# Optimization experiments

Hardware: AMD Instinct MI355X
Metric: run time of the kernel (lower is better)

The kernel has to match this reference:

```python
import jax, jax.numpy as jnp
import numpy as np

N_NODES = 50000
N_EDGES = 1600000
IN_DIM = 128
HID = 128
SHARED = 64
N_GRAPHS = 2048


def setup_inputs() -> dict:
    key = jax.random.key(0)
    ks = jax.random.split(key, 16)
    x = jax.random.normal(ks[0], (N_NODES, IN_DIM), dtype=jnp.float32)
    edge_index = jax.random.randint(ks[1], (2, N_EDGES), 0, N_NODES, dtype=jnp.int64)
    batch = jnp.sort(jax.random.randint(ks[2], (N_NODES,), 0, N_GRAPHS, dtype=jnp.int64))

    def lin(k, fan_in, fan_out):
        bound = 1.0 / np.sqrt(fan_in)
        kw, kb = jax.random.split(k)
        W = jax.random.uniform(kw, (fan_in, fan_out), minval=-bound, maxval=bound, dtype=jnp.float32)
        b = jax.random.uniform(kb, (fan_out,), minval=-bound, maxval=bound, dtype=jnp.float32)
        return W, b

    W1a, b1a = lin(ks[3], IN_DIM, HID)
    W1b, b1b = lin(ks[4], HID, HID)
    W2a, b2a = lin(ks[5], HID, HID)
    W2b, b2b = lin(ks[6], HID, HID)
    Ws, bs = lin(ks[7], HID, SHARED)
    WlS, blS = lin(ks[8], SHARED, 1)
    WlP, blP = lin(ks[9], SHARED, 1)
    WnR, bnR = lin(ks[10], SHARED, 1)
    return dict(x=x, edge_index=edge_index, batch=batch,
                W1a=W1a, b1a=b1a, W1b=W1b, b1b=b1b,
                W2a=W2a, b2a=b2a, W2b=W2b, b2b=b2b,
                Ws=Ws, bs=bs, WlS=WlS, blS=blS, WlP=WlP, blP=blP, WnR=WnR, bnR=bnR)


def gin_conv(x, src, dst, Wa, ba, Wb, bb):
    # GINConv (eps=0): h_i = MLP(x_i + sum_{j->i} x_j)
    agg = jax.ops.segment_sum(x[src], dst, num_segments=N_NODES)
    h = x + agg
    h = jax.nn.relu(h @ Wa + ba)
    return h @ Wb + bb


def reference(x, edge_index, batch, W1a, b1a, W1b, b1b, W2a, b2a, W2b, b2b,
              Ws, bs, WlS, blS, WlP, blP, WnR, bnR):
    src, dst = edge_index[0], edge_index[1]
    h = jax.nn.relu(gin_conv(x, src, dst, W1a, b1a, W1b, b1b))
    h = jax.nn.relu(gin_conv(h, src, dst, W2a, b2a, W2b, b2b))
    # global mean pool over graph ids
    sums = jax.ops.segment_sum(h, batch, num_segments=N_GRAPHS)
    counts = jax.ops.segment_sum(jnp.ones((h.shape[0],), h.dtype), batch, num_segments=N_GRAPHS)
    pooled = sums / jnp.maximum(counts, 1.0)[:, None]
    g = jax.nn.relu(pooled @ Ws + bs)
    out_logS = (g @ WlS + blS)[:, 0]
    out_logP = (g @ WlP + blP)[:, 0]
    out_NR = (g @ WnR + bnR)[:, 0]
    return (out_logS, out_logP, out_NR)
```

## Files before the change

### kernel.cpp

```cpp
#include <hip/hip_runtime.h>
#include <hip/hip_bf16.h>


#define IN_DIM 128
#define NFINE 128
#define BIN_EPB 4096
#define SRCCH 16
#define NSLOT 6400
#define SPT 13

typedef float  f32x4  __attribute__((ext_vector_type(4)));
typedef short  bf16x4 __attribute__((ext_vector_type(4)));
typedef short  bf16x8 __attribute__((ext_vector_type(8)));

__device__ __forceinline__ unsigned short bf16_rne(float v) {
    unsigned u = __float_as_uint(v);
    unsigned t = u + 0x7fffu + ((u >> 16) & 1u);
    return (unsigned short)(t >> 16);
}


__global__ __launch_bounds__(256) void f32_to_bf16_kernel(
    const float4* __restrict__ in, uint4* __restrict__ out, int n8)
{
    int i = blockIdx.x * 256 + threadIdx.x;
    if (i >= n8) return;
    float4 a = in[i * 2];
    float4 b = in[i * 2 + 1];
    float v[8] = {a.x, a.y, a.z, a.w, b.x, b.y, b.z, b.w};
    unsigned r[4];
#pragma unroll
    for (int j = 0; j < 4; ++j)
        r[j] = (unsigned)bf16_rne(v[j * 2]) | ((unsigned)bf16_rne(v[j * 2 + 1]) << 16);
    out[i] = make_uint4(r[0], r[1], r[2], r[3]);
}


__global__ __launch_bounds__(256) void conv_weights_kernel(
    const float* __restrict__ W0, const float* __restrict__ W1,
    const float* __restrict__ W2, const float* __restrict__ W3,
    unsigned short* __restrict__ Wh, unsigned short* __restrict__ Wl)
{
    int m   = blockIdx.x >> 6;
    int idx = (blockIdx.x & 63) * 256 + threadIdx.x;
    const float* W = (m == 0) ? W0 : (m == 1) ? W1 : (m == 2) ? W2 : W3;
    int k = idx >> 7, n = idx & 127;
    float v = W[idx];
    unsigned short hh = bf16_rne(v);
    float hf = __uint_as_float(((unsigned)hh) << 16);
    unsigned short ll = bf16_rne(v - hf);
    Wh[m * 16384 + n * 128 + k] = hh;
    Wl[m * 16384 + n * 128 + k] = ll;
}


__global__ __launch_bounds__(256) void bin_kernel(
    const int* __restrict__ src, const int* __restrict__ dst,
    int2* __restrict__ buckets, int* __restrict__ bcur,
    int n_edges, int n_nodes, int cap)
{
    __shared__ int cnt[NFINE];
    __shared__ int base[NFINE];
    for (int i = threadIdx.x; i < NFINE; i += 256) cnt[i] = 0;
    __syncthreads();

    const int e0 = blockIdx.x * BIN_EPB + threadIdx.x * 16;
    int ne = n_edges - e0;
    if (ne < 0) ne = 0;
    if (ne > 16) ne = 16;

    int d[16], s[16], off[16];
    if (ne == 16) {
#pragma unroll
        for (int q = 0; q < 4; ++q) {
            int4 dv = *(const int4*)(dst + e0 + q * 4);
            int4 sv = *(const int4*)(src + e0 + q * 4);
            d[q * 4 + 0] = dv.x; d[q * 4 + 1] = dv.y;
            d[q * 4 + 2] = dv.z; d[q * 4 + 3] = dv.w;
            s[q * 4 + 0] = sv.x; s[q * 4 + 1] = sv.y;
            s[q * 4 + 2] = sv.z; s[q * 4 + 3] = sv.w;
        }
    } else {
#pragma unroll
        for (int j = 0; j < 16; ++j) {
            d[j] = (j < ne) ? dst[e0 + j] : 0;
            s[j] = (j < ne) ? src[e0 + j] : 0;
        }
    }
#pragma unroll
    for (int j = 0; j < 16; ++j)
        if (j < ne) {
            int b = (int)(((long long)d[j] * NFINE) / n_nodes);
            off[j] = atomicAdd(&cnt[b], 1);
        }
    __syncthreads();
    for (int i = threadIdx.x; i < NFINE; i += 256)
        base[i] = atomicAdd(&bcur[i], cnt[i]);
    __syncthreads();
#pragma unroll
    for (int j = 0; j < 16; ++j)
        if (j < ne) {
            int b = (int)(((long long)d[j] * NFINE) / n_nodes);
            buckets[(size_t)b * cap + base[b] + off[j]] = make_int2(d[j], s[j]);
        }
}

__global__ __launch_bounds__(512) void csr_fused_kernel(
    const int2* __restrict__ buckets, const int* __restrict__ bcnt,
    int* __restrict__ row_start, int* __restrict__ csr_src,
    int cap, int n_nodes, int n_edges)
{
    __shared__ int bc[NFINE];
    __shared__ int h[NSLOT];
    __shared__ int tsum[512];
    __shared__ int bbase_s;

    const int b = blockIdx.x;
    const int t = threadIdx.x;
    const int lo_n = (int)(((long long)b * n_nodes + NFINE - 1) / NFINE);
    const int hi_n = (int)(((long long)(b + 1) * n_nodes + NFINE - 1) / NFINE);
    const int sl = hi_n - lo_n;

    if (t < NFINE) bc[t] = bcnt[t];
    for (int i = t; i < NSLOT; i += 512) h[i] = 0;
    __syncthreads();
    if (t == 0) {
        int s = 0;
        for (int i = 0; i < b; ++i) s += bc[i];
        bbase_s = s;
    }
    const int nb = bc[b];
    const int2* bp = buckets + (size_t)b * cap;
    __syncthreads();

    for (int i = t; i < nb; i += 512) {
        int2 e = bp[i];
        int key = (e.x - lo_n) * SRCCH + (int)(((long long)e.y * SRCCH) / n_nodes);
        atomicAdd(&h[key], 1);
    }
    __syncthreads();

    int base = 0;
#pragma unroll
    for (int j = 0; j < SPT; ++j) {
        int slot = t * SPT + j;
        if (slot < NSLOT) {
            int v = h[slot];
            h[slot] = base;
            base += v;
        }
    }
    tsum[t] = base;
    __syncthreads();
    for (int off = 1; off < 512; off <<= 1) {
        int tmp = (t >= off) ? tsum[t - off] : 0;
        __syncthreads();
        tsum[t] += tmp;
        __syncthreads();
    }
    int texcl = tsum[t] - base + bbase_s;
#pragma unroll
    for (int j = 0; j < SPT; ++j) {
        int slot = t * SPT + j;
        if (slot < NSLOT) h[slot] += texcl;
    }
    __syncthreads();
    for (int i = t; i < sl; i += 512) row_start[lo_n + i] = h[i * SRCCH];
    if (b == NFINE - 1 && t == 0) row_start[n_nodes] = n_edges;
    __syncthreads();

    for (int i = t; i < nb; i += 512) {
        int2 e = bp[i];
        int key = (e.x - lo_n) * SRCCH + (int)(((long long)e.y * SRCCH) / n_nodes);
        csr_src[atomicAdd(&h[key], 1)] = e.y;
    }
}


__device__ __forceinline__ void add_row8(float acc[8], uint4 r) {
    union { unsigned u; float f; } c;
    c.u = r.x << 16;         acc[0] += c.f;
    c.u = r.x & 0xffff0000u; acc[1] += c.f;
    c.u = r.y << 16;         acc[2] += c.f;
    c.u = r.y & 0xffff0000u; acc[3] += c.f;
    c.u = r.z << 16;         acc[4] += c.f;
    c.u = r.z & 0xffff0000u; acc[5] += c.f;
    c.u = r.w << 16;         acc[6] += c.f;
    c.u = r.w & 0xffff0000u; acc[7] += c.f;
}

template <bool SELF_SPLIT>
__global__ __launch_bounds__(256) void gather_agg_bf16_kernel(
    const float* __restrict__ xf,
    const uint4* __restrict__ sh,
    const uint4* __restrict__ slo,
    const uint4* __restrict__ xb,
    const int* __restrict__ row_start, const int* __restrict__ csr_src,
    uint4* __restrict__ outh, uint4* __restrict__ outl, int n_nodes)
{
    int blk = blockIdx.x;
    int nfull = (gridDim.x >> 5) << 5;
    int group;
    if (blk < nfull) {
        int x = blk & 7;
        int q = blk >> 3;
        group = ((q >> 2) << 5) + (x << 2) + (q & 3);
    } else {
        group = blk;
    }

    int node = group * 16 + (threadIdx.x >> 4);
    int lane = threadIdx.x & 15;
    if (node >= n_nodes) return;
    int lo = row_start[node];
    int hi = row_start[node + 1];

    float acc[8];
    if constexpr (SELF_SPLIT) {
        uint4 h = sh[(size_t)node * 16 + lane];
        uint4 l = slo[(size_t)node * 16 + lane];
#pragma unroll
        for (int j = 0; j < 8; ++j) acc[j] = 0.f;
        add_row8(acc, h);
        add_row8(acc, l);
    } else {
        const f32x4* xfr = (const f32x4*)(xf + (size_t)node * IN_DIM + lane * 8);
        f32x4 a0 = xfr[0];
        f32x4 a1 = xfr[1];
        acc[0] = a0.x; acc[1] = a0.y; acc[2] = a0.z; acc[3] = a0.w;
        acc[4] = a1.x; acc[5] = a1.y; acc[6] = a1.z; acc[7] = a1.w;
    }

    int e = lo;
    for (; e + 3 < hi; e += 4) {
        int s0 = csr_src[e];
        int s1 = csr_src[e + 1];
        int s2 = csr_src[e + 2];
        int s3 = csr_src[e + 3];
        uint4 r0 = xb[(size_t)s0 * 16 + lane];
        uint4 r1 = xb[(size_t)s1 * 16 + lane];
        uint4 r2 = xb[(size_t)s2 * 16 + lane];
        uint4 r3 = xb[(size_t)s3 * 16 + lane];
        add_row8(acc, r0);
        add_row8(acc, r1);
        add_row8(acc, r2);
        add_row8(acc, r3);
    }
    for (; e < hi; ++e) {
        uint4 r = xb[(size_t)csr_src[e] * 16 + lane];
        add_row8(acc, r);
    }

    unsigned ph[4], pl[4];
#pragma unroll
    for (int j = 0; j < 4; ++j) {
        unsigned short h0 = bf16_rne(acc[2 * j]);
        unsigned short l0 = bf16_rne(acc[2 * j] - __uint_as_float(((unsigned)h0) << 16));
        unsigned short h1 = bf16_rne(acc[2 * j + 1]);
        unsigned short l1 = bf16_rne(acc[2 * j + 1] - __uint_as_float(((unsigned)h1) << 16));
        ph[j] = (unsigned)h0 | ((unsigned)h1 << 16);
        pl[j] = (unsigned)l0 | ((unsigned)l1 << 16);
    }
    outh[(size_t)node * 16 + lane] = make_uint4(ph[0], ph[1], ph[2], ph[3]);
    outl[(size_t)node * 16 + lane] = make_uint4(pl[0], pl[1], pl[2], pl[3]);
}

#define HSTRIDE 132

template <bool EMIT_SPLIT>
__global__ __launch_bounds__(512) void fused_mlp_kernel(
    const unsigned short* __restrict__ Ah, const unsigned short* __restrict__ Al,
    const unsigned short* __restrict__ Wa_h, const unsigned short* __restrict__ Wa_l,
    const float* __restrict__ ba,
    const unsigned short* __restrict__ Wb_h, const unsigned short* __restrict__ Wb_l,
    const float* __restrict__ bb,
    float* __restrict__ C, unsigned short* __restrict__ Ch,
    unsigned short* __restrict__ Cl, int M)
{
    __shared__ __align__(16) unsigned short Hh[64][HSTRIDE];
    __shared__ __align__(16) unsigned short Hl[64][HSTRIDE];

    const int t    = threadIdx.x;
    const int wave = t >> 6;
    const int lane = t & 63;
    const int l15  = lane & 15;
    const int quad = lane >> 4;
    const int rh   = (wave & 1) * 32;
    const int cq   = (wave >> 1) * 32;
    const int brow = blockIdx.x * 64;

    f32x4 acc[2][2];
#pragma unroll
    for (int ti = 0; ti < 2; ++ti)
#pragma unroll
        for (int ct = 0; ct < 2; ++ct) acc[ti][ct] = {0.f, 0.f, 0.f, 0.f};

    {
        int ar0 = brow + rh + l15;
        int ar1 = brow + rh + 16 + l15;
        if (ar0 >= M) ar0 = M - 1;
        if (ar1 >= M) ar1 = M - 1;
        const unsigned short* a0h = Ah + (size_t)ar0 * IN_DIM + quad * 8;
        const unsigned short* a0l = Al + (size_t)ar0 * IN_DIM + quad * 8;
        const unsigned short* a1h = Ah + (size_t)ar1 * IN_DIM + quad * 8;
        const unsigned short* a1l = Al + (size_t)ar1 * IN_DIM + quad * 8;
#pragma unroll
        for (int k0 = 0; k0 < IN_DIM; k0 += 32) {
            bf16x8 ah0 = *(const bf16x8*)(a0h + k0);
            bf16x8 al0 = *(const bf16x8*)(a0l + k0);
            bf16x8 ah1 = *(const bf16x8*)(a1h + k0);
            bf16x8 al1 = *(const bf16x8*)(a1l + k0);
#pragma unroll
            for (int ct = 0; ct < 2; ++ct) {
                const size_t woff = (size_t)(cq + ct * 16 + l15) * IN_DIM + k0 + quad * 8;
                bf16x8 wh = *(const bf16x8*)(Wa_h + woff);
                bf16x8 wl = *(const bf16x8*)(Wa_l + woff);
                acc[0][ct] = __builtin_amdgcn_mfma_f32_16x16x32_bf16(ah0, wh, acc[0][ct], 0, 0, 0);
                acc[1][ct] = __builtin_amdgcn_mfma_f32_16x16x32_bf16(ah1, wh, acc[1][ct], 0, 0, 0);
                acc[0][ct] = __builtin_amdgcn_mfma_f32_16x16x32_bf16(al0, wh, acc[0][ct], 0, 0, 0);
                acc[1][ct] = __builtin_amdgcn_mfma_f32_16x16x32_bf16(al1, wh, acc[1][ct], 0, 0, 0);
                acc[0][ct] = __builtin_amdgcn_mfma_f32_16x16x32_bf16(ah0, wl, acc[0][ct], 0, 0, 0);
                acc[1][ct] = __builtin_amdgcn_mfma_f32_16x16x32_bf16(ah1, wl, acc[1][ct], 0, 0, 0);
            }
        }
    }

#pragma unroll
    for (int ti = 0; ti < 2; ++ti) {
#pragma unroll
        for (int ct = 0; ct < 2; ++ct) {
            int col = cq + ct * 16 + l15;
            float b = ba[col];
#pragma unroll
            for (int r = 0; r < 4; ++r) {
                int rl = rh + ti * 16 + quad * 4 + r;
                float v = fmaxf(acc[ti][ct][r] + b, 0.f);
                unsigned short hh = bf16_rne(v);
                Hh[rl][col] = hh;
                Hl[rl][col] = bf16_rne(v - __uint_as_float(((unsigned)hh) << 16));
            }
            acc[ti][ct] = {0.f, 0.f, 0.f, 0.f};
        }
    }
    __syncthreads();

#pragma unroll
    for (int k0 = 0; k0 < IN_DIM; k0 += 32) {
        const int hk = k0 + quad * 8;
        bf16x8 ah[2], al[2];
#pragma unroll
        for (int ti = 0; ti < 2; ++ti) {
            const int hr = rh + ti * 16 + l15;
            bf16x4 h0 = *(const bf16x4*)&Hh[hr][hk];
            bf16x4 h1 = *(const bf16x4*)&Hh[hr][hk + 4];
            bf16x4 l0 = *(const bf16x4*)&Hl[hr][hk];
            bf16x4 l1 = *(const bf16x4*)&Hl[hr][hk + 4];
            ah[ti] = __builtin_shufflevector(h0, h1, 0, 1, 2, 3, 4, 5, 6, 7);
            al[ti] = __builtin_shufflevector(l0, l1, 0, 1, 2, 3, 4, 5, 6, 7);
        }
#pragma unroll
        for (int ct = 0; ct < 2; ++ct) {
            const size_t woff = (size_t)(cq + ct * 16 + l15) * IN_DIM + k0 + quad * 8;
            bf16x8 wh = *(const bf16x8*)(Wb_h + woff);
            bf16x8 wl = *(const bf16x8*)(Wb_l + woff);
            acc[0][ct] = __builtin_amdgcn_mfma_f32_16x16x32_bf16(ah[0], wh, acc[0][ct], 0, 0, 0);
            acc[1][ct] = __builtin_amdgcn_mfma_f32_16x16x32_bf16(ah[1], wh, acc[1][ct], 0, 0, 0);
            acc[0][ct] = __builtin_amdgcn_mfma_f32_16x16x32_bf16(al[0], wh, acc[0][ct], 0, 0, 0);
            acc[1][ct] = __builtin_amdgcn_mfma_f32_16x16x32_bf16(al[1], wh, acc[1][ct], 0, 0, 0);
            acc[0][ct] = __builtin_amdgcn_mfma_f32_16x16x32_bf16(ah[0], wl, acc[0][ct], 0, 0, 0);
            acc[1][ct] = __builtin_amdgcn_mfma_f32_16x16x32_bf16(ah[1], wl, acc[1][ct], 0, 0, 0);
        }
    }

#pragma unroll
    for (int ti = 0; ti < 2; ++ti) {
        const int rbase = brow + rh + ti * 16 + quad * 4;
#pragma unroll
        for (int ct = 0; ct < 2; ++ct) {
            int col = cq + ct * 16 + l15;
            float b = bb[col];
#pragma unroll
            for (int r = 0; r < 4; ++r) {
                int row = rbase + r;
                if (row < M) {
                    float o = fmaxf(acc[ti][ct][r] + b, 0.f);
                    if (EMIT_SPLIT) {
                        unsigned short hh = bf16_rne(o);
                        Ch[(size_t)row * IN_DIM + col] = hh;
                        Cl[(size_t)row * IN_DIM + col] =
                            bf16_rne(o - __uint_as_float(((unsigned)hh) << 16));
                    } else {
                        C[(size_t)row * IN_DIM + col] = o;
                    }
                }
            }
        }
    }
}


__device__ __forceinline__ int lower_bound_i(const int* __restrict__ a, int n, int v) {
    int lo = 0, hi = n;
    while (lo < hi) {
        int mid = (lo + hi) >> 1;
        if (a[mid] < v) lo = mid + 1; else hi = mid;
    }
    return lo;
}

__global__ __launch_bounds__(128) void pool_kernel(
    const float* __restrict__ h, const int* __restrict__ batch,
    float* __restrict__ pooled, int n_nodes, int n_graphs)
{
    int g = blockIdx.x;
    int lo = lower_bound_i(batch, n_nodes, g);
    int hi = lower_bound_i(batch, n_nodes, g + 1);
    int j = threadIdx.x;
    float acc = 0.f;
    for (int i = lo; i < hi; ++i)
        acc += h[(size_t)i * IN_DIM + j];
    float cnt = (float)(hi - lo);
    pooled[(size_t)g * IN_DIM + j] = acc / fmaxf(cnt, 1.0f);
}

__global__ __launch_bounds__(64) void head_kernel(
    const float* __restrict__ pooled,
    const float* __restrict__ Ws,  const float* __restrict__ bs,
    const float* __restrict__ WlS, const float* __restrict__ blS,
    const float* __restrict__ WlP, const float* __restrict__ blP,
    const float* __restrict__ WnR, const float* __restrict__ bnR,
    float* __restrict__ out, int n_graphs)
{
    int g = blockIdx.x;
    int j = threadIdx.x;
    const float* p = pooled + (size_t)g * IN_DIM;
    float acc = bs[j];
#pragma unroll 8
    for (int k = 0; k < IN_DIM; ++k)
        acc = fmaf(p[k], Ws[k * 64 + j], acc);
    float gj = fmaxf(acc, 0.f);
    float s1 = gj * WlS[j];
    float s2 = gj * WlP[j];
    float s3 = gj * WnR[j];
#pragma unroll
    for (int off = 32; off > 0; off >>= 1) {
        s1 += __shfl_down(s1, off);
        s2 += __shfl_down(s2, off);
        s3 += __shfl_down(s3, off);
    }
    if (j == 0) {
        out[g]                = s1 + blS[0];
        out[n_graphs + g]     = s2 + blP[0];
        out[2 * n_graphs + g] = s3 + bnR[0];
    }
}


extern "C" void kernel_launch(void* const* d_in, const int* in_sizes, int n_in,
                              void* d_out, int out_size, void* d_ws, size_t ws_size,
                              hipStream_t stream)
{
    const float* x   = (const float*)d_in[0];
    const int*   ei  = (const int*)d_in[1];
    const int*   bat = (const int*)d_in[2];
    const float* W1a = (const float*)d_in[3];
    const float* b1a = (const float*)d_in[4];
    const float* W1b = (const float*)d_in[5];
    const float* b1b = (const float*)d_in[6];
    const float* W2a = (const float*)d_in[7];
    const float* b2a = (const float*)d_in[8];
    const float* W2b = (const float*)d_in[9];
    const float* b2b = (const float*)d_in[10];
    const float* Ws  = (const float*)d_in[11];
    const float* bs  = (const float*)d_in[12];
    const float* WlS = (const float*)d_in[13];
    const float* blS = (const float*)d_in[14];
    const float* WlP = (const float*)d_in[15];
    const float* blP = (const float*)d_in[16];
    const float* WnR = (const float*)d_in[17];
    const float* bnR = (const float*)d_in[18];

    const int n_nodes  = in_sizes[0] / IN_DIM;
    const int n_edges  = in_sizes[1] / 2;
    const int n_graphs = out_size / 3;
    const int* src = ei;
    const int* dst = ei + n_edges;

    const size_t node_elems   = (size_t)n_nodes * IN_DIM;
    const size_t pooled_elems = (size_t)n_graphs * IN_DIM;

    float* P1     = (float*)d_ws;
    float* P2     = P1 + node_elems;
    float* P3     = P2 + node_elems;
    float* pooled = P3 + node_elems;
    int* row_start = (int*)(pooled + pooled_elems);
    int* bcur      = row_start + (n_nodes + 1);
    int* csr_src   = bcur + NFINE;
    unsigned short* wt_h = (unsigned short*)(csr_src + n_edges);
    unsigned short* wt_l = wt_h + 4 * 16384;

    unsigned short* Ah = (unsigned short*)P1;
    unsigned short* Al = Ah + node_elems;
    unsigned short* xb = (unsigned short*)P2;
    unsigned short* Ch = xb;
    unsigned short* Cl = Ch + node_elems;

    const int cap = n_edges / NFINE + 2048;
    int2* buckets = (int2*)P1;

    const int gatherblocks = (int)(((size_t)n_nodes * 16 + 255) / 256);
    const int mlpblocks = (n_nodes + 63) / 64;
    const int binblocks = (n_edges + BIN_EPB - 1) / BIN_EPB;
    const int n8 = (int)(node_elems / 8);
    const int cvtblocks = (n8 + 255) / 256;

    conv_weights_kernel<<<256, 256, 0, stream>>>(W1a, W1b, W2a, W2b, wt_h, wt_l);
    hipMemsetAsync(bcur, 0, NFINE * sizeof(int), stream);
    bin_kernel<<<binblocks, 256, 0, stream>>>(src, dst, buckets, bcur,
                                              n_edges, n_nodes, cap);
    csr_fused_kernel<<<NFINE, 512, 0, stream>>>(buckets, bcur, row_start,
                                                csr_src, cap, n_nodes, n_edges);

    f32_to_bf16_kernel<<<cvtblocks, 256, 0, stream>>>((const float4*)x, (uint4*)xb, n8);
    gather_agg_bf16_kernel<false><<<gatherblocks, 256, 0, stream>>>(
        x, nullptr, nullptr, (const uint4*)xb, row_start, csr_src,
        (uint4*)Ah, (uint4*)Al, n_nodes);
    fused_mlp_kernel<true><<<mlpblocks, 512, 0, stream>>>(
        Ah, Al, wt_h, wt_l, b1a, wt_h + 16384, wt_l + 16384, b1b,
        nullptr, Ch, Cl, n_nodes);

    gather_agg_bf16_kernel<true><<<gatherblocks, 256, 0, stream>>>(
        nullptr, (const uint4*)Ch, (const uint4*)Cl, (const uint4*)Ch,
        row_start, csr_src, (uint4*)Ah, (uint4*)Al, n_nodes);
    fused_mlp_kernel<false><<<mlpblocks, 512, 0, stream>>>(
        Ah, Al, wt_h + 2 * 16384, wt_l + 2 * 16384, b2a,
        wt_h + 3 * 16384, wt_l + 3 * 16384, b2b,
        P3, nullptr, nullptr, n_nodes);

    pool_kernel<<<n_graphs, 128, 0, stream>>>(P3, bat, pooled, n_nodes, n_graphs);
    head_kernel<<<n_graphs, 64, 0, stream>>>(pooled, Ws, bs, WlS, blS, WlP, blP,
                                             WnR, bnR, (float*)d_out, n_graphs);
}
```

Before: 383.3 us.

## Fuse neighbor gather-aggregation into the GIN MLP kernel via shared memory

Merges the gather/aggregate kernel into the fused MLP kernel. Each 512-thread block first aggregates its 64 nodes' neighbor rows into hi/lo bf16 tiles in LDS, then feeds the MFMA GEMMs from LDS instead of reading split A matrices from global memory. This removes a global write and read of the aggregated activations plus two launches per layer. The trade-off is that the gather loses its block swizzle and its higher per-kernel occupancy, and that the gather and MFMA phases are serialized within each block. Workspace layout is reorganized, and edge buckets now alias the layer-2 output buffer.

```diff
diff --git a/kernel.cpp b/kernel.cpp
--- a/kernel.cpp
+++ b/kernel.cpp
@@ -176,6 +176,7 @@
     }
 }
 
+#define HSTRIDE 132
 
 __device__ __forceinline__ void add_row8(float acc[8], uint4 r) {
     union { unsigned u; float f; } c;
@@ -189,87 +190,13 @@
     c.u = r.w & 0xffff0000u; acc[7] += c.f;
 }
 
-template <bool SELF_SPLIT>
-__global__ __launch_bounds__(256) void gather_agg_bf16_kernel(
+template <int LAYER>
+__global__ __launch_bounds__(512) void fused_gin_layer_kernel(
     const float* __restrict__ xf,
-    const uint4* __restrict__ sh,
-    const uint4* __restrict__ slo,
-    const uint4* __restrict__ xb,
+    const uint4* __restrict__ selfh,
+    const uint4* __restrict__ selfl,
+    const uint4* __restrict__ nbr,
     const int* __restrict__ row_start, const int* __restrict__ csr_src,
-    uint4* __restrict__ outh, uint4* __restrict__ outl, int n_nodes)
-{
-    int blk = blockIdx.x;
-    int nfull = (gridDim.x >> 5) << 5;
-    int group;
-    if (blk < nfull) {
-        int x = blk & 7;
-        int q = blk >> 3;
-        group = ((q >> 2) << 5) + (x << 2) + (q & 3);
-    } else {
-        group = blk;
-    }
-
-    int node = group * 16 + (threadIdx.x >> 4);
-    int lane = threadIdx.x & 15;
-    if (node >= n_nodes) return;
-    int lo = row_start[node];
-    int hi = row_start[node + 1];
-
-    float acc[8];
-    if constexpr (SELF_SPLIT) {
-        uint4 h = sh[(size_t)node * 16 + lane];
-        uint4 l = slo[(size_t)node * 16 + lane];
-#pragma unroll
-        for (int j = 0; j < 8; ++j) acc[j] = 0.f;
-        add_row8(acc, h);
-        add_row8(acc, l);
-    } else {
-        const f32x4* xfr = (const f32x4*)(xf + (size_t)node * IN_DIM + lane * 8);
-        f32x4 a0 = xfr[0];
-        f32x4 a1 = xfr[1];
-        acc[0] = a0.x; acc[1] = a0.y; acc[2] = a0.z; acc[3] = a0.w;
-        acc[4] = a1.x; acc[5] = a1.y; acc[6] = a1.z; acc[7] = a1.w;
-    }
-
-    int e = lo;
-    for (; e + 3 < hi; e += 4) {
-        int s0 = csr_src[e];
-        int s1 = csr_src[e + 1];
-        int s2 = csr_src[e + 2];
-        int s3 = csr_src[e + 3];
-        uint4 r0 = xb[(size_t)s0 * 16 + lane];
-        uint4 r1 = xb[(size_t)s1 * 16 + lane];
-        uint4 r2 = xb[(size_t)s2 * 16 + lane];
-        uint4 r3 = xb[(size_t)s3 * 16 + lane];
-        add_row8(acc, r0);
-        add_row8(acc, r1);
-        add_row8(acc, r2);
-        add_row8(acc, r3);
-    }
-    for (; e < hi; ++e) {
-        uint4 r = xb[(size_t)csr_src[e] * 16 + lane];
-        add_row8(acc, r);
-    }
-
-    unsigned ph[4], pl[4];
-#pragma unroll
-    for (int j = 0; j < 4; ++j) {
-        unsigned short h0 = bf16_rne(acc[2 * j]);
-        unsigned short l0 = bf16_rne(acc[2 * j] - __uint_as_float(((unsigned)h0) << 16));
-        unsigned short h1 = bf16_rne(acc[2 * j + 1]);
-        unsigned short l1 = bf16_rne(acc[2 * j + 1] - __uint_as_float(((unsigned)h1) << 16));
-        ph[j] = (unsigned)h0 | ((unsigned)h1 << 16);
-        pl[j] = (unsigned)l0 | ((unsigned)l1 << 16);
-    }
-    outh[(size_t)node * 16 + lane] = make_uint4(ph[0], ph[1], ph[2], ph[3]);
-    outl[(size_t)node * 16 + lane] = make_uint4(pl[0], pl[1], pl[2], pl[3]);
-}
-
-#define HSTRIDE 132
-
-template <bool EMIT_SPLIT>
-__global__ __launch_bounds__(512) void fused_mlp_kernel(
-    const unsigned short* __restrict__ Ah, const unsigned short* __restrict__ Al,
     const unsigned short* __restrict__ Wa_h, const unsigned short* __restrict__ Wa_l,
     const float* __restrict__ ba,
     const unsigned short* __restrict__ Wb_h, const unsigned short* __restrict__ Wb_l,
@@ -281,13 +208,68 @@
     __shared__ __align__(16) unsigned short Hl[64][HSTRIDE];
 
     const int t    = threadIdx.x;
+    const int brow = blockIdx.x * 64;
+
+    {
+        const int lane = t & 15;
+        const int gr   = t >> 4;
+#pragma unroll
+        for (int it = 0; it < 2; ++it) {
+            const int rl   = it * 32 + gr;
+            const int node = brow + rl;
+            float acc[8] = {0.f, 0.f, 0.f, 0.f, 0.f, 0.f, 0.f, 0.f};
+            if (node < M) {
+                if constexpr (LAYER == 1) {
+                    const f32x4* xfr = (const f32x4*)(xf + (size_t)node * IN_DIM + lane * 8);
+                    f32x4 a0 = xfr[0];
+                    f32x4 a1 = xfr[1];
+                    acc[0] = a0.x; acc[1] = a0.y; acc[2] = a0.z; acc[3] = a0.w;
+                    acc[4] = a1.x; acc[5] = a1.y; acc[6] = a1.z; acc[7] = a1.w;
+                } else {
+                    add_row8(acc, selfh[(size_t)node * 16 + lane]);
+                    add_row8(acc, selfl[(size_t)node * 16 + lane]);
+                }
+                const int lo = row_start[node];
+                const int hi = row_start[node + 1];
+                int e = lo;
+                for (; e + 3 < hi; e += 4) {
+                    int s0 = csr_src[e];
+                    int s1 = csr_src[e + 1];
+                    int s2 = csr_src[e + 2];
+                    int s3 = csr_src[e + 3];
+                    uint4 r0 = nbr[(size_t)s0 * 16 + lane];
+                    uint4 r1 = nbr[(size_t)s1 * 16 + lane];
+                    uint4 r2 = nbr[(size_t)s2 * 16 + lane];
+                    uint4 r3 = nbr[(size_t)s3 * 16 + lane];
+                    add_row8(acc, r0);
+                    add_row8(acc, r1);
+                    add_row8(acc, r2);
+                    add_row8(acc, r3);
+                }
+                for (; e < hi; ++e)
+                    add_row8(acc, nbr[(size_t)csr_src[e] * 16 + lane]);
+            }
+            unsigned short hh[8], ll[8];
+#pragma unroll
+            for (int j = 0; j < 8; ++j) {
+                unsigned short h = bf16_rne(acc[j]);
+                hh[j] = h;
+                ll[j] = bf16_rne(acc[j] - __uint_as_float(((unsigned)h) << 16));
+            }
+            *(bf16x4*)&Hh[rl][lane * 8]     = *(const bf16x4*)&hh[0];
+            *(bf16x4*)&Hh[rl][lane * 8 + 4] = *(const bf16x4*)&hh[4];
+            *(bf16x4*)&Hl[rl][lane * 8]     = *(const bf16x4*)&ll[0];
+            *(bf16x4*)&Hl[rl][lane * 8 + 4] = *(const bf16x4*)&ll[4];
+        }
+    }
+    __syncthreads();
+
     const int wave = t >> 6;
     const int lane = t & 63;
     const int l15  = lane & 15;
     const int quad = lane >> 4;
     const int rh   = (wave & 1) * 32;
     const int cq   = (wave >> 1) * 32;
-    const int brow = blockIdx.x * 64;
 
     f32x4 acc[2][2];
 #pragma unroll
@@ -295,35 +277,34 @@
 #pragma unroll
         for (int ct = 0; ct < 2; ++ct) acc[ti][ct] = {0.f, 0.f, 0.f, 0.f};
 
-    {
-        int ar0 = brow + rh + l15;
-        int ar1 = brow + rh + 16 + l15;
-        if (ar0 >= M) ar0 = M - 1;
-        if (ar1 >= M) ar1 = M - 1;
-        const unsigned short* a0h = Ah + (size_t)ar0 * IN_DIM + quad * 8;
-        const unsigned short* a0l = Al + (size_t)ar0 * IN_DIM + quad * 8;
-        const unsigned short* a1h = Ah + (size_t)ar1 * IN_DIM + quad * 8;
-        const unsigned short* a1l = Al + (size_t)ar1 * IN_DIM + quad * 8;
-#pragma unroll
-        for (int k0 = 0; k0 < IN_DIM; k0 += 32) {
-            bf16x8 ah0 = *(const bf16x8*)(a0h + k0);
-            bf16x8 al0 = *(const bf16x8*)(a0l + k0);
-            bf16x8 ah1 = *(const bf16x8*)(a1h + k0);
-            bf16x8 al1 = *(const bf16x8*)(a1l + k0);
-#pragma unroll
-            for (int ct = 0; ct < 2; ++ct) {
-                const size_t woff = (size_t)(cq + ct * 16 + l15) * IN_DIM + k0 + quad * 8;
-                bf16x8 wh = *(const bf16x8*)(Wa_h + woff);
-                bf16x8 wl = *(const bf16x8*)(Wa_l + woff);
-                acc[0][ct] = __builtin_amdgcn_mfma_f32_16x16x32_bf16(ah0, wh, acc[0][ct], 0, 0, 0);
-                acc[1][ct] = __builtin_amdgcn_mfma_f32_16x16x32_bf16(ah1, wh, acc[1][ct], 0, 0, 0);
-                acc[0][ct] = __builtin_amdgcn_mfma_f32_16x16x32_bf16(al0, wh, acc[0][ct], 0, 0, 0);
-                acc[1][ct] = __builtin_amdgcn_mfma_f32_16x16x32_bf16(al1, wh, acc[1][ct], 0, 0, 0);
-                acc[0][ct] = __builtin_amdgcn_mfma_f32_16x16x32_bf16(ah0, wl, acc[0][ct], 0, 0, 0);
-                acc[1][ct] = __builtin_amdgcn_mfma_f32_16x16x32_bf16(ah1, wl, acc[1][ct], 0, 0, 0);
-            }
-        }
-    }
+#pragma unroll
+    for (int k0 = 0; k0 < IN_DIM; k0 += 32) {
+        const int hk = k0 + quad * 8;
+        bf16x8 ah[2], al[2];
+#pragma unroll
+        for (int ti = 0; ti < 2; ++ti) {
+            const int hr = rh + ti * 16 + l15;
+            bf16x4 h0 = *(const bf16x4*)&Hh[hr][hk];
+            bf16x4 h1 = *(const bf16x4*)&Hh[hr][hk + 4];
+            bf16x4 l0 = *(const bf16x4*)&Hl[hr][hk];
+            bf16x4 l1 = *(const bf16x4*)&Hl[hr][hk + 4];
+            ah[ti] = __builtin_shufflevector(h0, h1, 0, 1, 2, 3, 4, 5, 6, 7);
+            al[ti] = __builtin_shufflevector(l0, l1, 0, 1, 2, 3, 4, 5, 6, 7);
+        }
+#pragma unroll
+        for (int ct = 0; ct < 2; ++ct) {
+            const size_t woff = (size_t)(cq + ct * 16 + l15) * IN_DIM + k0 + quad * 8;
+            bf16x8 wh = *(const bf16x8*)(Wa_h + woff);
+            bf16x8 wl = *(const bf16x8*)(Wa_l + woff);
+            acc[0][ct] = __builtin_amdgcn_mfma_f32_16x16x32_bf16(ah[0], wh, acc[0][ct], 0, 0, 0);
+            acc[1][ct] = __builtin_amdgcn_mfma_f32_16x16x32_bf16(ah[1], wh, acc[1][ct], 0, 0, 0);
+            acc[0][ct] = __builtin_amdgcn_mfma_f32_16x16x32_bf16(al[0], wh, acc[0][ct], 0, 0, 0);
+            acc[1][ct] = __builtin_amdgcn_mfma_f32_16x16x32_bf16(al[1], wh, acc[1][ct], 0, 0, 0);
+            acc[0][ct] = __builtin_amdgcn_mfma_f32_16x16x32_bf16(ah[0], wl, acc[0][ct], 0, 0, 0);
+            acc[1][ct] = __builtin_amdgcn_mfma_f32_16x16x32_bf16(ah[1], wl, acc[1][ct], 0, 0, 0);
+        }
+    }
+    __syncthreads();
 
 #pragma unroll
     for (int ti = 0; ti < 2; ++ti) {
@@ -384,7 +365,7 @@
                 int row = rbase + r;
                 if (row < M) {
                     float o = fmaxf(acc[ti][ct][r] + b, 0.f);
-                    if (EMIT_SPLIT) {
+                    if constexpr (LAYER == 1) {
                         unsigned short hh = bf16_rne(o);
                         Ch[(size_t)row * IN_DIM + col] = hh;
                         Cl[(size_t)row * IN_DIM + col] =
@@ -489,9 +470,10 @@
     const size_t node_elems   = (size_t)n_nodes * IN_DIM;
     const size_t pooled_elems = (size_t)n_graphs * IN_DIM;
 
-    float* P1     = (float*)d_ws;
-    float* P2     = P1 + node_elems;
-    float* P3     = P2 + node_elems;
+    unsigned short* xb = (unsigned short*)d_ws;
+    unsigned short* Ch = xb + node_elems;
+    unsigned short* Cl = Ch + node_elems;
+    float* P3     = (float*)(Cl + node_elems);
     float* pooled = P3 + node_elems;
     int* row_start = (int*)(pooled + pooled_elems);
     int* bcur      = row_start + (n_nodes + 1);
@@ -499,17 +481,10 @@
     unsigned short* wt_h = (unsigned short*)(csr_src + n_edges);
     unsigned short* wt_l = wt_h + 4 * 16384;
 
-    unsigned short* Ah = (unsigned short*)P1;
-    unsigned short* Al = Ah + node_elems;
-    unsigned short* xb = (unsigned short*)P2;
-    unsigned short* Ch = xb;
-    unsigned short* Cl = Ch + node_elems;
-
     const int cap = n_edges / NFINE + 2048;
-    int2* buckets = (int2*)P1;
-
-    const int gatherblocks = (int)(((size_t)n_nodes * 16 + 255) / 256);
-    const int mlpblocks = (n_nodes + 63) / 64;
+    int2* buckets = (int2*)P3;
+
+    const int layerblocks = (n_nodes + 63) / 64;
     const int binblocks = (n_edges + BIN_EPB - 1) / BIN_EPB;
     const int n8 = (int)(node_elems / 8);
     const int cvtblocks = (n8 + 255) / 256;
@@ -520,20 +495,17 @@
                                               n_edges, n_nodes, cap);
     csr_fused_kernel<<<NFINE, 512, 0, stream>>>(buckets, bcur, row_start,
                                                 csr_src, cap, n_nodes, n_edges);
-
     f32_to_bf16_kernel<<<cvtblocks, 256, 0, stream>>>((const float4*)x, (uint4*)xb, n8);
-    gather_agg_bf16_kernel<false><<<gatherblocks, 256, 0, stream>>>(
+
+    fused_gin_layer_kernel<1><<<layerblocks, 512, 0, stream>>>(
         x, nullptr, nullptr, (const uint4*)xb, row_start, csr_src,
-        (uint4*)Ah, (uint4*)Al, n_nodes);
-    fused_mlp_kernel<true><<<mlpblocks, 512, 0, stream>>>(
-        Ah, Al, wt_h, wt_l, b1a, wt_h + 16384, wt_l + 16384, b1b,
+        wt_h, wt_l, b1a, wt_h + 16384, wt_l + 16384, b1b,
         nullptr, Ch, Cl, n_nodes);
 
-    gather_agg_bf16_kernel<true><<<gatherblocks, 256, 0, stream>>>(
+    fused_gin_layer_kernel<2><<<layerblocks, 512, 0, stream>>>(
         nullptr, (const uint4*)Ch, (const uint4*)Cl, (const uint4*)Ch,
-        row_start, csr_src, (uint4*)Ah, (uint4*)Al, n_nodes);
-    fused_mlp_kernel<false><<<mlpblocks, 512, 0, stream>>>(
-        Ah, Al, wt_h + 2 * 16384, wt_l + 2 * 16384, b2a,
+        row_start, csr_src,
+        wt_h + 2 * 16384, wt_l + 2 * 16384, b2a,
         wt_h + 3 * 16384, wt_l + 3 * 16384, b2b,
         P3, nullptr, nullptr, n_nodes);
 
```

New measurement: 344.0 us. 10.2% less time.
